# Performance work log

Measured on AMD Instinct MI355X. Metric: run time of the kernel, lower is better.

## Reference

```python
import jax, jax.numpy as jnp
import numpy as np

B, N, IC, PC, OUT = 2, 4096, 256, 128, 128
BN_EPS = 1e-5


def setup_inputs() -> dict:
    key = jax.random.key(0)
    ks = jax.random.split(key, 6)
    return {
        "point_features": jax.random.normal(ks[0], (B, PC, N), jnp.float32),
        "img_features": jax.random.normal(ks[1], (B, IC, N), jnp.float32),
        "fc2_w": jax.random.normal(ks[2], (PC, IC), jnp.float32) * (1.0 / np.sqrt(IC)),
        "fc2_b": jax.random.normal(ks[3], (PC,), jnp.float32) * 0.01,
        "conv_w": jax.random.normal(ks[4], (OUT, 2 * PC), jnp.float32) * (1.0 / np.sqrt(2 * PC)),
        "conv_b": jax.random.normal(ks[5], (OUT,), jnp.float32) * 0.01,
        "bn_gamma": jnp.ones((OUT,), jnp.float32),
        "bn_beta": jnp.zeros((OUT,), jnp.float32),
        "bn_mean": jnp.zeros((OUT,), jnp.float32),
        "bn_var": jnp.ones((OUT,), jnp.float32),
    }


def reference(point_features, img_features, fc2_w, fc2_b, conv_w, conv_b,
              bn_gamma, bn_beta, bn_mean, bn_var):
    # IA_layer3 (dropout in eval mode -> identity)
    rp = jnp.swapaxes(point_features, 1, 2)            # [B, N, pc]
    ri = jnp.swapaxes(img_features, 1, 2) @ fc2_w.T + fc2_b  # fc2: [B, N, pc]
    scale = 1.0 / np.sqrt(PC).astype(np.float32)

    # scores = rp @ ri^T / sqrt(d); softmax over dim=1 (the rp-token axis)
    s_p = jnp.einsum('bnd,bmd->bnm', rp, ri) * scale   # [B, N, N]
    aw_p = jax.nn.softmax(s_p, axis=1)
    out_p = jnp.einsum('bij,bjd->bid', aw_p, rp)       # [B, N, pc]

    s_i = jnp.einsum('bnd,bmd->bnm', ri, rp) * scale   # [B, N, N]
    aw_i = jax.nn.softmax(s_i, axis=1)
    out_i = jnp.einsum('bij,bjd->bid', aw_i, ri)       # [B, N, pc]

    # fuse: permute to channel-first, concat on channels -> [B, 2*pc, N]
    fusion = jnp.concatenate([jnp.swapaxes(out_p, 1, 2),
                              jnp.swapaxes(out_i, 1, 2)], axis=1)
    # conv1d(k=1) + BN(eval) + ReLU, all per-channel elementwise over N
    y = jnp.einsum('oc,bcn->bon', conv_w, fusion) + conv_b[None, :, None]
    inv_std = jax.lax.rsqrt(bn_var + BN_EPS)
    y = (y - bn_mean[None, :, None]) * (bn_gamma * inv_std)[None, :, None] \
        + bn_beta[None, :, None]
    return jax.nn.relu(y)                              # [B, OUT, N]
```

## Files before the change

kernel.cpp:

```cpp
#include <hip/hip_runtime.h>
#include <math.h>

#define NTOK 4096
#define PCH  128
#define ICH  256
#define OCH  128
#define NB   2
#define SCALEF 0.08838834764831845f

typedef __bf16 bf16_t;
typedef __attribute__((ext_vector_type(8))) __bf16 bf16x8;
typedef __attribute__((ext_vector_type(4))) __bf16 bf16x4;
typedef __attribute__((ext_vector_type(4))) float floatx4;

#define LDK 136
#define LDJ 72

__global__ __launch_bounds__(256) void zero_kernel(float4* __restrict__ p)
{
    p[(size_t)blockIdx.x * 256 + threadIdx.x] = float4{0.f, 0.f, 0.f, 0.f};
}

__global__ __launch_bounds__(256) void pack_pf(const float* __restrict__ pf,
                                               bf16_t* __restrict__ pfC,
                                               bf16_t* __restrict__ pfT)
{
    __shared__ float Ls[64][65];
    const int t = threadIdx.x;
    const int n0 = blockIdx.x * 64, d0 = blockIdx.y * 64, b = blockIdx.z;
    const float* src = pf + ((size_t)(b * PCH + d0)) * NTOK + n0;
#pragma unroll
    for (int p = 0; p < 4; p++) {
        int d = p * 16 + (t >> 4), c = t & 15;
        float4 v = *(const float4*)&src[d * NTOK + c * 4];
        Ls[d][c * 4 + 0] = v.x; Ls[d][c * 4 + 1] = v.y;
        Ls[d][c * 4 + 2] = v.z; Ls[d][c * 4 + 3] = v.w;
        bf16x4 o = { (bf16_t)v.x, (bf16_t)v.y, (bf16_t)v.z, (bf16_t)v.w };
        *(bf16x4*)&pfC[((size_t)(b * PCH + d0 + d)) * NTOK + n0 + c * 4] = o;
    }
    __syncthreads();
#pragma unroll
    for (int p = 0; p < 2; p++) {
        int n = p * 32 + (t >> 3), c = t & 7;
        bf16x8 o;
#pragma unroll
        for (int k = 0; k < 8; k++) o[k] = (bf16_t)Ls[c * 8 + k][n];
        *(bf16x8*)&pfT[((size_t)(b * NTOK + n0 + n)) * PCH + d0 + c * 8] = o;
    }
}

__global__ __launch_bounds__(256) void pack_img(const float* __restrict__ img,
                                                bf16_t* __restrict__ imgT)
{
    __shared__ float Ls[64][65];
    const int t = threadIdx.x;
    const int n0 = blockIdx.x * 64, c0 = blockIdx.y * 64, b = blockIdx.z;
    const float* src = img + ((size_t)(b * ICH + c0)) * NTOK + n0;
#pragma unroll
    for (int p = 0; p < 4; p++) {
        int d = p * 16 + (t >> 4), c = t & 15;
        float4 v = *(const float4*)&src[d * NTOK + c * 4];
        Ls[d][c * 4 + 0] = v.x; Ls[d][c * 4 + 1] = v.y;
        Ls[d][c * 4 + 2] = v.z; Ls[d][c * 4 + 3] = v.w;
    }
    __syncthreads();
#pragma unroll
    for (int p = 0; p < 2; p++) {
        int n = p * 32 + (t >> 3), c = t & 7;
        bf16x8 o;
#pragma unroll
        for (int k = 0; k < 8; k++) o[k] = (bf16_t)Ls[c * 8 + k][n];
        *(bf16x8*)&imgT[((size_t)(b * NTOK + n0 + n)) * ICH + c0 + c * 8] = o;
    }
}

__global__ __launch_bounds__(256) void fc2_mfma(const bf16_t* __restrict__ imgT,
                                                const float* __restrict__ w,
                                                const float* __restrict__ bias,
                                                bf16_t* __restrict__ riC,
                                                bf16_t* __restrict__ riT)
{
    const int t = threadIdx.x;
    const int n0 = blockIdx.x * 64, pbase = blockIdx.y * 64, b = blockIdx.z;
    const int lane = t & 63, wv = t >> 6, tx = lane & 15, q = lane >> 4;
    const int n = n0 + wv * 16 + tx;
    const bf16_t* trow = imgT + ((size_t)(b * NTOK + n)) * ICH;

    floatx4 acc[4];
#pragma unroll
    for (int ot = 0; ot < 4; ot++) acc[ot] = (floatx4){0.f, 0.f, 0.f, 0.f};

#pragma unroll
    for (int s = 0; s < 8; s++) {
        bf16x8 bf = *(const bf16x8*)&trow[s * 32 + q * 8];
#pragma unroll
        for (int ot = 0; ot < 4; ot++) {
            const float* wr = w + (size_t)(pbase + ot * 16 + tx) * ICH + s * 32 + q * 8;
            float4 x0 = *(const float4*)wr;
            float4 x1 = *(const float4*)(wr + 4);
            bf16x8 af;
            af[0] = (bf16_t)x0.x; af[1] = (bf16_t)x0.y; af[2] = (bf16_t)x0.z; af[3] = (bf16_t)x0.w;
            af[4] = (bf16_t)x1.x; af[5] = (bf16_t)x1.y; af[6] = (bf16_t)x1.z; af[7] = (bf16_t)x1.w;
            acc[ot] = __builtin_amdgcn_mfma_f32_16x16x32_bf16(af, bf, acc[ot], 0, 0, 0);
        }
    }

#pragma unroll
    for (int ot = 0; ot < 4; ot++) {
        bf16x4 tv;
#pragma unroll
        for (int r = 0; r < 4; r++) {
            const int p = pbase + ot * 16 + q * 4 + r;
            float v = acc[ot][r] + bias[p];
            tv[r] = (bf16_t)v;
            riC[((size_t)(b * PCH + p)) * NTOK + n] = (bf16_t)v;
        }
        *(bf16x4*)&riT[((size_t)(b * NTOK + n)) * PCH + pbase + ot * 16 + q * 4] = tv;
    }
}

__global__ __launch_bounds__(256, 4) void stats_mfma(const bf16_t* __restrict__ pfT,
                                                     const bf16_t* __restrict__ riT,
                                                     float* __restrict__ zr,
                                                     float* __restrict__ zc)
{
    __shared__ bf16_t As[64 * LDK];
    __shared__ float zacc[1024];
    const int b = blockIdx.y, t = threadIdx.x;
    const int js = blockIdx.z;
    const bf16_t* At = pfT + (size_t)b * NTOK * PCH;
    const bf16_t* Bt = riT + (size_t)b * NTOK * PCH;
    float* zrow = zr + (size_t)b * NTOK;
    float* zcol = zc + (size_t)b * NTOK;
    const int lane = t & 63, w = t >> 6, tx = lane & 15, q = lane >> 4;
    const int i0 = blockIdx.x * 64;
    const int jbase = js * 1024;
    const int sr = t >> 4, sc = t & 15;
    const bf16_t* Brow = Bt + (size_t)(jbase + w * 16 + tx) * PCH;

    bf16x8 bcur[4];
#pragma unroll
    for (int s = 0; s < 4; s++)
        bcur[s] = *(const bf16x8*)&Brow[s * 32 + q * 8];
#pragma unroll
    for (int p = 0; p < 4; p++) {
        int i = p * 16 + sr;
        *(uint4*)&As[i * LDK + sc * 8] = *(const uint4*)&At[((size_t)(i0 + i)) * PCH + sc * 8];
    }
    __syncthreads();
    bf16x8 af[4][4];
#pragma unroll
    for (int mt = 0; mt < 4; mt++)
#pragma unroll
        for (int s = 0; s < 4; s++)
            af[mt][s] = *(bf16x8*)&As[(mt * 16 + tx) * LDK + s * 32 + q * 8];

    float racc[4] = {0.f, 0.f, 0.f, 0.f};
    for (int jt = 0; jt < 16; jt++) {
        __builtin_amdgcn_s_barrier();
        floatx4 sacc[4];
#pragma unroll
        for (int mt = 0; mt < 4; mt++) {
            sacc[mt] = (floatx4){0.f, 0.f, 0.f, 0.f};
#pragma unroll
            for (int s = 0; s < 4; s++)
                sacc[mt] = __builtin_amdgcn_mfma_f32_16x16x32_bf16(bcur[s], af[mt][s], sacc[mt], 0, 0, 0);
        }
        if (jt < 15) {
            const bf16_t* bn = Brow + (size_t)(jt + 1) * 64 * PCH;
#pragma unroll
            for (int s = 0; s < 4; s++)
                bcur[s] = *(const bf16x8*)&bn[s * 32 + q * 8];
        }

        float ctmp[4] = {0.f, 0.f, 0.f, 0.f};
#pragma unroll
        for (int mt = 0; mt < 4; mt++)
#pragma unroll
            for (int r = 0; r < 4; r++) {
                float e = __expf(sacc[mt][r] * SCALEF);
                racc[mt] += e;
                ctmp[r]  += e;
            }
#pragma unroll
        for (int r = 0; r < 4; r++) {
            float v = ctmp[r];
            v += __shfl_xor(v, 1); v += __shfl_xor(v, 2);
            v += __shfl_xor(v, 4); v += __shfl_xor(v, 8);
            if (tx == 0) zacc[jt * 64 + w * 16 + q * 4 + r] = v;
        }
    }
#pragma unroll
    for (int mt = 0; mt < 4; mt++) {
        float v = racc[mt];
        v += __shfl_xor(v, 16);
        v += __shfl_xor(v, 32);
        if (q == 0) atomicAdd(&zrow[i0 + mt * 16 + tx], v);
    }
    __syncthreads();
#pragma unroll
    for (int k = 0; k < 4; k++)
        atomicAdd(&zcol[jbase + k * 256 + t], zacc[k * 256 + t]);
}

__global__ __launch_bounds__(256, 3) void attn_mfma(const bf16_t* __restrict__ pfT,
                                                    const bf16_t* __restrict__ riT,
                                                    const bf16_t* __restrict__ pfC,
                                                    const bf16_t* __restrict__ riC,
                                                    const float* __restrict__ zrsum,
                                                    const float* __restrict__ zcsum,
                                                    float* __restrict__ fus)
{
    __shared__ bf16_t As[64 * LDK];
    __shared__ bf16_t Es[2][64 * LDJ];
    const int b = blockIdx.y, t = threadIdx.x;
    const int mode = blockIdx.z >> 2, js = blockIdx.z & 3;
    const bf16_t* At = (mode == 0 ? pfT : riT) + (size_t)b * NTOK * PCH;
    const bf16_t* Bt = (mode == 0 ? riT : pfT) + (size_t)b * NTOK * PCH;
    const bf16_t* Vc = (mode == 0 ? pfC : riC) + (size_t)b * PCH * NTOK;
    const float* wsum = (mode == 0 ? zcsum : zrsum) + (size_t)b * NTOK;
    const int lane = t & 63, w = t >> 6, tx = lane & 15, q = lane >> 4;
    const int i0 = blockIdx.x * 64;
    const int jbase = js * 1024;
    const int sr = t >> 4, sc = t & 15;
    const bf16_t* Brow = Bt + (size_t)(jbase + w * 16 + tx) * PCH;

    bf16x8 bcur[4];
#pragma unroll
    for (int s = 0; s < 4; s++)
        bcur[s] = *(const bf16x8*)&Brow[s * 32 + q * 8];
    bf16x8 vcur[2][2];
#pragma unroll
    for (int nt = 0; nt < 2; nt++)
#pragma unroll
        for (int s = 0; s < 2; s++)
            vcur[nt][s] = *(const bf16x8*)&Vc[((size_t)(w * 32 + nt * 16 + tx)) * NTOK + jbase + s * 32 + q * 8];
    float4 wv = *(const float4*)&wsum[jbase + w * 16 + q * 4];
    float4 wr4 = {1.f / wv.x, 1.f / wv.y, 1.f / wv.z, 1.f / wv.w};

#pragma unroll
    for (int p = 0; p < 4; p++) {
        int i = p * 16 + sr;
        *(uint4*)&As[i * LDK + sc * 8] = *(const uint4*)&At[((size_t)(i0 + i)) * PCH + sc * 8];
    }
    __syncthreads();
    bf16x8 af[4][4];
#pragma unroll
    for (int mt = 0; mt < 4; mt++)
#pragma unroll
        for (int s = 0; s < 4; s++)
            af[mt][s] = *(bf16x8*)&As[(mt * 16 + tx) * LDK + s * 32 + q * 8];

    floatx4 outacc[4][2];
#pragma unroll
    for (int mt = 0; mt < 4; mt++)
#pragma unroll
        for (int nt = 0; nt < 2; nt++)
            outacc[mt][nt] = (floatx4){0.f, 0.f, 0.f, 0.f};

    for (int jt = 0; jt < 16; jt++) {
        const int cur = jt & 1;
        const int j0 = jbase + jt * 64;

        floatx4 sacc[4];
#pragma unroll
        for (int mt = 0; mt < 4; mt++) {
            sacc[mt] = (floatx4){0.f, 0.f, 0.f, 0.f};
#pragma unroll
            for (int s = 0; s < 4; s++)
                sacc[mt] = __builtin_amdgcn_mfma_f32_16x16x32_bf16(bcur[s], af[mt][s], sacc[mt], 0, 0, 0);
        }
        if (jt < 15) {
            const bf16_t* bn = Brow + (size_t)(jt + 1) * 64 * PCH;
#pragma unroll
            for (int s = 0; s < 4; s++)
                bcur[s] = *(const bf16x8*)&bn[s * 32 + q * 8];
        }

#pragma unroll
        for (int mt = 0; mt < 4; mt++) {
            bf16x4 ev;
#pragma unroll
            for (int r = 0; r < 4; r++)
                ev[r] = (bf16_t)(__expf(sacc[mt][r] * SCALEF) * ((const float*)&wr4)[r]);
            *(bf16x4*)&Es[cur][(mt * 16 + tx) * LDJ + w * 16 + q * 4] = ev;
        }
        float4 wnv;
        if (jt < 15)
            wnv = *(const float4*)&wsum[j0 + 64 + w * 16 + q * 4];

        __syncthreads();

        bf16x8 ef[4][2];
#pragma unroll
        for (int mt = 0; mt < 4; mt++)
#pragma unroll
            for (int s = 0; s < 2; s++)
                ef[mt][s] = *(bf16x8*)&Es[cur][(mt * 16 + tx) * LDJ + s * 32 + q * 8];
#pragma unroll
        for (int nt = 0; nt < 2; nt++)
#pragma unroll
            for (int s = 0; s < 2; s++)
#pragma unroll
                for (int mt = 0; mt < 4; mt++)
                    outacc[mt][nt] = __builtin_amdgcn_mfma_f32_16x16x32_bf16(ef[mt][s], vcur[nt][s], outacc[mt][nt], 0, 0, 0);

        if (jt < 15) {
#pragma unroll
            for (int nt = 0; nt < 2; nt++)
#pragma unroll
                for (int s = 0; s < 2; s++)
                    vcur[nt][s] = *(const bf16x8*)&Vc[((size_t)(w * 32 + nt * 16 + tx)) * NTOK + (j0 + 64) + s * 32 + q * 8];
            wr4 = (float4){1.f / wnv.x, 1.f / wnv.y, 1.f / wnv.z, 1.f / wnv.w};
        }
    }

    float* fo = fus + ((size_t)(b * NTOK + i0)) * 256 + mode * 128 + w * 32;
#pragma unroll
    for (int mt = 0; mt < 4; mt++)
#pragma unroll
        for (int nt = 0; nt < 2; nt++)
#pragma unroll
            for (int r = 0; r < 4; r++)
                atomicAdd(&fo[(mt * 16 + q * 4 + r) * 256 + nt * 16 + tx], outacc[mt][nt][r]);
}

__global__ __launch_bounds__(256) void conv_mfma(const float* __restrict__ fus,
                                                 const float* __restrict__ cw,
                                                 const float* __restrict__ cb,
                                                 const float* __restrict__ g,
                                                 const float* __restrict__ be,
                                                 const float* __restrict__ mu,
                                                 const float* __restrict__ var,
                                                 float* __restrict__ out)
{
    const int t = threadIdx.x;
    const int n0 = blockIdx.x * 64, obase = blockIdx.y * 64, b = blockIdx.z;
    const int lane = t & 63, wv = t >> 6, tx = lane & 15, q = lane >> 4;
    const int n = n0 + wv * 16 + tx;
    const float* frow = fus + ((size_t)(b * NTOK + n)) * 256;

    floatx4 acc[4];
#pragma unroll
    for (int ot = 0; ot < 4; ot++) acc[ot] = (floatx4){0.f, 0.f, 0.f, 0.f};

#pragma unroll
    for (int s = 0; s < 8; s++) {
        float4 f0 = *(const float4*)&frow[s * 32 + q * 8];
        float4 f1 = *(const float4*)&frow[s * 32 + q * 8 + 4];
        bf16x8 bf;
        bf[0] = (bf16_t)f0.x; bf[1] = (bf16_t)f0.y; bf[2] = (bf16_t)f0.z; bf[3] = (bf16_t)f0.w;
        bf[4] = (bf16_t)f1.x; bf[5] = (bf16_t)f1.y; bf[6] = (bf16_t)f1.z; bf[7] = (bf16_t)f1.w;
#pragma unroll
        for (int ot = 0; ot < 4; ot++) {
            const float* wr = cw + (size_t)(obase + ot * 16 + tx) * 256 + s * 32 + q * 8;
            float4 x0 = *(const float4*)wr;
            float4 x1 = *(const float4*)(wr + 4);
            bf16x8 af;
            af[0] = (bf16_t)x0.x; af[1] = (bf16_t)x0.y; af[2] = (bf16_t)x0.z; af[3] = (bf16_t)x0.w;
            af[4] = (bf16_t)x1.x; af[5] = (bf16_t)x1.y; af[6] = (bf16_t)x1.z; af[7] = (bf16_t)x1.w;
            acc[ot] = __builtin_amdgcn_mfma_f32_16x16x32_bf16(af, bf, acc[ot], 0, 0, 0);
        }
    }

#pragma unroll
    for (int ot = 0; ot < 4; ot++)
#pragma unroll
        for (int r = 0; r < 4; r++) {
            const int o = obase + ot * 16 + q * 4 + r;
            const float sc = g[o] * rsqrtf(var[o] + 1e-5f);
            const float b0 = be[o] + (cb[o] - mu[o]) * sc;
            float y = acc[ot][r] * sc + b0;
            out[((size_t)(b * OCH + o)) * NTOK + n] = fmaxf(y, 0.f);
        }
}

extern "C" void kernel_launch(void* const* d_in, const int* in_sizes, int n_in,
                              void* d_out, int out_size, void* d_ws, size_t ws_size,
                              hipStream_t stream)
{
    const float* pf   = (const float*)d_in[0];
    const float* img  = (const float*)d_in[1];
    const float* fc2w = (const float*)d_in[2];
    const float* fc2b = (const float*)d_in[3];
    const float* cw   = (const float*)d_in[4];
    const float* cb   = (const float*)d_in[5];
    const float* g    = (const float*)d_in[6];
    const float* be   = (const float*)d_in[7];
    const float* mu   = (const float*)d_in[8];
    const float* var  = (const float*)d_in[9];
    float* out = (float*)d_out;

    float* fus   = (float*)d_ws;
    float* zrsum = fus + (size_t)NB * NTOK * 256;
    float* zcsum = zrsum + NB * NTOK;
    bf16_t* pfC = (bf16_t*)(zcsum + NB * NTOK);
    bf16_t* pfT = pfC + (size_t)NB * PCH * NTOK;
    bf16_t* riC = pfT + (size_t)NB * NTOK * PCH;
    bf16_t* riT = riC + (size_t)NB * PCH * NTOK;
    bf16_t* imgT = (bf16_t*)fus;

    pack_pf    <<<dim3(64, 2, NB),  256, 0, stream>>>(pf, pfC, pfT);
    pack_img   <<<dim3(64, 4, NB),  256, 0, stream>>>(img, imgT);
    fc2_mfma   <<<dim3(64, 2, NB),  256, 0, stream>>>(imgT, fc2w, fc2b, riC, riT);
    zero_kernel<<<dim3(2064), 256, 0, stream>>>((float4*)d_ws);
    stats_mfma <<<dim3(64, NB, 4),  256, 0, stream>>>(pfT, riT, zrsum, zcsum);
    attn_mfma  <<<dim3(64, NB, 8),  256, 0, stream>>>(pfT, riT, pfC, riC, zrsum, zcsum, fus);
    conv_mfma  <<<dim3(64, 2, NB),  256, 0, stream>>>(fus, cw, cb, g, be, mu, var, out);
}
```

Baseline: 214.1 us.

## Merge pack kernels, fold zeroing into later kernels, swizzle blocks per XCD

Merges the two input-packing kernels into one launch and drops the standalone zero kernel. The score-sum buffers are now zeroed inside fc2, and the fusion buffer is zeroed inside the stats kernel. The stats and attention grids become 1D with an index remap, so blocks that share a batch and key-slice are launched with the same value of blockIdx mod 8. The intent is to keep their shared K/V tiles resident in one XCD's L2 and to save launch overhead. The zeroing depends on exact grid sizes matching buffer sizes, and it relies on imgT (which aliases fus) being consumed by fc2 before stats runs.

```diff
diff --git a/kernel.cpp b/kernel.cpp
--- a/kernel.cpp
+++ b/kernel.cpp
@@ -16,27 +16,29 @@
 #define LDK 136
 #define LDJ 72
 
-__global__ __launch_bounds__(256) void zero_kernel(float4* __restrict__ p)
-{
-    p[(size_t)blockIdx.x * 256 + threadIdx.x] = float4{0.f, 0.f, 0.f, 0.f};
-}
-
-__global__ __launch_bounds__(256) void pack_pf(const float* __restrict__ pf,
-                                               bf16_t* __restrict__ pfC,
-                                               bf16_t* __restrict__ pfT)
+__global__ __launch_bounds__(256) void pack_all(const float* __restrict__ pf,
+                                                const float* __restrict__ img,
+                                                bf16_t* __restrict__ pfC,
+                                                bf16_t* __restrict__ pfT,
+                                                bf16_t* __restrict__ imgT)
 {
     __shared__ float Ls[64][65];
     const int t = threadIdx.x;
-    const int n0 = blockIdx.x * 64, d0 = blockIdx.y * 64, b = blockIdx.z;
-    const float* src = pf + ((size_t)(b * PCH + d0)) * NTOK + n0;
+    const int n0 = blockIdx.x * 64, b = blockIdx.z;
+    const bool ispf = blockIdx.y < 2;
+    const int d0 = ispf ? blockIdx.y * 64 : (blockIdx.y - 2) * 64;
+    const float* src = (ispf ? pf + ((size_t)(b * PCH + d0)) * NTOK
+                             : img + ((size_t)(b * ICH + d0)) * NTOK) + n0;
 #pragma unroll
     for (int p = 0; p < 4; p++) {
         int d = p * 16 + (t >> 4), c = t & 15;
         float4 v = *(const float4*)&src[d * NTOK + c * 4];
         Ls[d][c * 4 + 0] = v.x; Ls[d][c * 4 + 1] = v.y;
         Ls[d][c * 4 + 2] = v.z; Ls[d][c * 4 + 3] = v.w;
-        bf16x4 o = { (bf16_t)v.x, (bf16_t)v.y, (bf16_t)v.z, (bf16_t)v.w };
-        *(bf16x4*)&pfC[((size_t)(b * PCH + d0 + d)) * NTOK + n0 + c * 4] = o;
+        if (ispf) {
+            bf16x4 o = { (bf16_t)v.x, (bf16_t)v.y, (bf16_t)v.z, (bf16_t)v.w };
+            *(bf16x4*)&pfC[((size_t)(b * PCH + d0 + d)) * NTOK + n0 + c * 4] = o;
+        }
     }
     __syncthreads();
 #pragma unroll
@@ -45,32 +47,10 @@
         bf16x8 o;
 #pragma unroll
         for (int k = 0; k < 8; k++) o[k] = (bf16_t)Ls[c * 8 + k][n];
-        *(bf16x8*)&pfT[((size_t)(b * NTOK + n0 + n)) * PCH + d0 + c * 8] = o;
-    }
-}
-
-__global__ __launch_bounds__(256) void pack_img(const float* __restrict__ img,
-                                                bf16_t* __restrict__ imgT)
-{
-    __shared__ float Ls[64][65];
-    const int t = threadIdx.x;
-    const int n0 = blockIdx.x * 64, c0 = blockIdx.y * 64, b = blockIdx.z;
-    const float* src = img + ((size_t)(b * ICH + c0)) * NTOK + n0;
-#pragma unroll
-    for (int p = 0; p < 4; p++) {
-        int d = p * 16 + (t >> 4), c = t & 15;
-        float4 v = *(const float4*)&src[d * NTOK + c * 4];
-        Ls[d][c * 4 + 0] = v.x; Ls[d][c * 4 + 1] = v.y;
-        Ls[d][c * 4 + 2] = v.z; Ls[d][c * 4 + 3] = v.w;
-    }
-    __syncthreads();
-#pragma unroll
-    for (int p = 0; p < 2; p++) {
-        int n = p * 32 + (t >> 3), c = t & 7;
-        bf16x8 o;
-#pragma unroll
-        for (int k = 0; k < 8; k++) o[k] = (bf16_t)Ls[c * 8 + k][n];
-        *(bf16x8*)&imgT[((size_t)(b * NTOK + n0 + n)) * ICH + c0 + c * 8] = o;
+        if (ispf)
+            *(bf16x8*)&pfT[((size_t)(b * NTOK + n0 + n)) * PCH + d0 + c * 8] = o;
+        else
+            *(bf16x8*)&imgT[((size_t)(b * NTOK + n0 + n)) * ICH + d0 + c * 8] = o;
     }
 }
 
@@ -78,9 +58,13 @@
                                                 const float* __restrict__ w,
                                                 const float* __restrict__ bias,
                                                 bf16_t* __restrict__ riC,
-                                                bf16_t* __restrict__ riT)
+                                                bf16_t* __restrict__ riT,
+                                                float* __restrict__ zsums)
 {
     const int t = threadIdx.x;
+    if (blockIdx.y == 0 && blockIdx.z == 0)
+        zsums[blockIdx.x * 256 + t] = 0.f;
+
     const int n0 = blockIdx.x * 64, pbase = blockIdx.y * 64, b = blockIdx.z;
     const int lane = t & 63, wv = t >> 6, tx = lane & 15, q = lane >> 4;
     const int n = n0 + wv * 16 + tx;
@@ -122,18 +106,30 @@
 __global__ __launch_bounds__(256, 4) void stats_mfma(const bf16_t* __restrict__ pfT,
                                                      const bf16_t* __restrict__ riT,
                                                      float* __restrict__ zr,
-                                                     float* __restrict__ zc)
+                                                     float* __restrict__ zc,
+                                                     float* __restrict__ fus)
 {
     __shared__ bf16_t As[64 * LDK];
     __shared__ float zacc[1024];
-    const int b = blockIdx.y, t = threadIdx.x;
-    const int js = blockIdx.z;
+    const int t = threadIdx.x;
+    const int blk = blockIdx.x;
+
+    {
+        float4* f4 = (float4*)fus + ((size_t)blk * 256 + t) * 4;
+        f4[0] = float4{0.f, 0.f, 0.f, 0.f};
+        f4[1] = float4{0.f, 0.f, 0.f, 0.f};
+        f4[2] = float4{0.f, 0.f, 0.f, 0.f};
+        f4[3] = float4{0.f, 0.f, 0.f, 0.f};
+    }
+
+    const int g = blk & 7, slot = blk >> 3;
+    const int b = g & 1, js = g >> 1;
     const bf16_t* At = pfT + (size_t)b * NTOK * PCH;
     const bf16_t* Bt = riT + (size_t)b * NTOK * PCH;
     float* zrow = zr + (size_t)b * NTOK;
     float* zcol = zc + (size_t)b * NTOK;
     const int lane = t & 63, w = t >> 6, tx = lane & 15, q = lane >> 4;
-    const int i0 = blockIdx.x * 64;
+    const int i0 = slot * 64;
     const int jbase = js * 1024;
     const int sr = t >> 4, sc = t & 15;
     const bf16_t* Brow = Bt + (size_t)(jbase + w * 16 + tx) * PCH;
@@ -213,14 +209,18 @@
 {
     __shared__ bf16_t As[64 * LDK];
     __shared__ bf16_t Es[2][64 * LDJ];
-    const int b = blockIdx.y, t = threadIdx.x;
-    const int mode = blockIdx.z >> 2, js = blockIdx.z & 3;
+    const int t = threadIdx.x;
+    const int blk = blockIdx.x;
+    const int g = (blk & 7) * 2 + ((blk >> 3) >> 6);
+    const int slot = (blk >> 3) & 63;
+    const int b = g & 1, z = g >> 1;
+    const int mode = z >> 2, js = z & 3;
     const bf16_t* At = (mode == 0 ? pfT : riT) + (size_t)b * NTOK * PCH;
     const bf16_t* Bt = (mode == 0 ? riT : pfT) + (size_t)b * NTOK * PCH;
     const bf16_t* Vc = (mode == 0 ? pfC : riC) + (size_t)b * PCH * NTOK;
     const float* wsum = (mode == 0 ? zcsum : zrsum) + (size_t)b * NTOK;
     const int lane = t & 63, w = t >> 6, tx = lane & 15, q = lane >> 4;
-    const int i0 = blockIdx.x * 64;
+    const int i0 = slot * 64;
     const int jbase = js * 1024;
     const int sr = t >> 4, sc = t & 15;
     const bf16_t* Brow = Bt + (size_t)(jbase + w * 16 + tx) * PCH;
@@ -400,11 +400,9 @@
     bf16_t* riT = riC + (size_t)NB * PCH * NTOK;
     bf16_t* imgT = (bf16_t*)fus;
 
-    pack_pf    <<<dim3(64, 2, NB),  256, 0, stream>>>(pf, pfC, pfT);
-    pack_img   <<<dim3(64, 4, NB),  256, 0, stream>>>(img, imgT);
-    fc2_mfma   <<<dim3(64, 2, NB),  256, 0, stream>>>(imgT, fc2w, fc2b, riC, riT);
-    zero_kernel<<<dim3(2064), 256, 0, stream>>>((float4*)d_ws);
-    stats_mfma <<<dim3(64, NB, 4),  256, 0, stream>>>(pfT, riT, zrsum, zcsum);
-    attn_mfma  <<<dim3(64, NB, 8),  256, 0, stream>>>(pfT, riT, pfC, riC, zrsum, zcsum, fus);
-    conv_mfma  <<<dim3(64, 2, NB),  256, 0, stream>>>(fus, cw, cb, g, be, mu, var, out);
-}
+    pack_all  <<<dim3(64, 6, NB), 256, 0, stream>>>(pf, img, pfC, pfT, imgT);
+    fc2_mfma  <<<dim3(64, 2, NB), 256, 0, stream>>>(imgT, fc2w, fc2b, riC, riT, zrsum);
+    stats_mfma<<<dim3(512),       256, 0, stream>>>(pfT, riT, zrsum, zcsum, fus);
+    attn_mfma <<<dim3(1024),      256, 0, stream>>>(pfT, riT, pfC, riC, zrsum, zcsum, fus);
+    conv_mfma <<<dim3(64, 2, NB), 256, 0, stream>>>(fus, cw, cb, g, be, mu, var, out);
+}
```

Measured after the change: 211.5 us. Within noise of the previous version (-1.2%).
